# Optimization experiments

Measured on AMD Instinct MI355X. Metric: run time of the kernel, lower is better.

The kernel has to match this reference:

```python
import jax, jax.numpy as jnp
import numpy as np
from jax import lax

N = 65536          # num nodes
D_IN = 512         # in_size
H = 128            # hidden_dim
TOP_K = 8
TEMP = 1.0
CHUNK = 512        # batch_size for streaming the similarity matrix


def setup_inputs() -> dict:
    key = jax.random.key(0)
    k1, k2, k3 = jax.random.split(key, 3)
    x = jax.random.normal(k1, (N, D_IN), dtype=jnp.float32)
    # xavier-ish scale for linear weights
    s = (2.0 / (D_IN + H)) ** 0.5
    Wq = jax.random.normal(k2, (D_IN, H), dtype=jnp.float32) * s
    Wk = jax.random.normal(k3, (D_IN, H), dtype=jnp.float32) * s
    bq = jnp.zeros((H,), dtype=jnp.float32)
    bk = jnp.zeros((H,), dtype=jnp.float32)
    return {"x": x, "Wq": Wq, "bq": bq, "Wk": Wk, "bk": bk}


def reference(x, Wq, bq, Wk, bk):
    """Attention-based kNN rewiring: per-node QK similarity + top-k neighbor selection.

    Streams the [N, N] similarity matrix in row-chunks of CHUNK (mirrors the
    torch batch loop) so only a [CHUNK, N] block is live at a time.
    Returns (topk_scores [N, K], dst_indices [N, K]); src of edge e for node i
    is simply i (edge_index = stack([arange(N).repeat(K), dst.ravel()])).
    """
    q = x @ Wq + bq                      # [N, H]
    k = x @ Wk + bk                      # [N, H]
    kT = k.T                             # [H, N]
    q_chunks = q.reshape(N // CHUNK, CHUNK, H)

    def chunk_fn(qb):
        sim = (qb @ kT) / TEMP           # [CHUNK, N]
        vals, idx = lax.top_k(sim, TOP_K)  # [CHUNK, K] each
        return vals, idx

    vals, idx = lax.map(chunk_fn, q_chunks)     # [N/CHUNK, CHUNK, K]
    return vals.reshape(N, TOP_K), idx.reshape(N, TOP_K)
```

## Files before the change

### kernel.cpp

```cpp
#include <hip/hip_runtime.h>
#include <stdint.h>


#define N_NODES 65536
#define D_IN    512
#define H_DIM   128
#define TOPK    8
#define NCH     24
#define NC      48
#define CTILE   128
#define NT      (N_NODES / CTILE)
#define NTH     (NT / 2)
#define RTILE   128
#define WS_REQ  ((size_t)88080384)

typedef __attribute__((ext_vector_type(8))) int   int8v;
typedef __attribute__((ext_vector_type(4))) int   int4v;
typedef __attribute__((ext_vector_type(4))) float float4_;

__device__ __forceinline__ unsigned f2fp8(float f) {
  const unsigned u = __float_as_uint(f);
  const unsigned s = (u >> 24) & 0x80u;
  const unsigned r = u + 0x0007FFFFu + ((u >> 20) & 1u);
  const int e = (int)((r >> 23) & 0xFFu) - 127;
  const unsigned m = (r >> 20) & 7u;
  if (e < -6) {
    float a = __builtin_fabsf(f);
    unsigned q = (unsigned)(a * 512.f + 0.5f);
    if (q > 7u) q = 7u;
    return s | q;
  }
  if (e > 8 || (e == 8 && m > 6u)) return s | 0x7Eu;
  return s | ((unsigned)(e + 7) << 3) | m;
}

__device__ __forceinline__ unsigned med3u(unsigned a, unsigned b, unsigned c) {
  unsigned d;
  asm("v_med3_u32 %0, %1, %2, %3" : "=v"(d) : "v"(a), "v"(b), "v"(c));
  return d;
}

#define INS8M(T, P) do {                                                       \
    const unsigned _p = (P);                                                   \
    T[7] = med3u(_p, T[6], T[7]);                                              \
    T[6] = med3u(_p, T[5], T[6]);                                              \
    T[5] = med3u(_p, T[4], T[5]);                                              \
    T[4] = med3u(_p, T[3], T[4]);                                              \
    T[3] = med3u(_p, T[2], T[3]);                                              \
    T[2] = med3u(_p, T[1], T[2]);                                              \
    T[1] = med3u(_p, T[0], T[1]);                                              \
    T[0] = (T[0] > _p) ? T[0] : _p;                                            \
  } while (0)

__device__ __forceinline__ void gload_lds16(const void* g, void* l) {
  typedef __attribute__((address_space(1))) const unsigned int gu32;
  typedef __attribute__((address_space(3))) unsigned int lu32;
  __builtin_amdgcn_global_load_lds((gu32*)(uintptr_t)g,
                                   (lu32*)(uint32_t)(uintptr_t)l, 16, 0, 0);
}

__global__ __launch_bounds__(256) void proj_kernel(
    const float* __restrict__ x,
    const float* __restrict__ Wq, const float* __restrict__ bq,
    const float* __restrict__ Wk, const float* __restrict__ bk,
    float* __restrict__ q32, float* __restrict__ k32)
{
  const int tid = threadIdx.x;
  const int rowbase = blockIdx.x * 32;
  const int c = tid;
  const float* Wcol = (c < 128) ? (Wq + c) : (Wk + (c - 128));
  const float bias  = (c < 128) ? bq[c] : bk[c - 128];
  const float* xrow = x + (size_t)rowbase * D_IN;

  float acc[32];
  #pragma unroll
  for (int r = 0; r < 32; ++r) acc[r] = 0.f;

  for (int kc = 0; kc < D_IN; kc += 16) {
    float wv[16];
    #pragma unroll
    for (int u = 0; u < 16; ++u) wv[u] = Wcol[(size_t)(kc + u) * H_DIM];
    #pragma unroll
    for (int r = 0; r < 32; ++r) {
      #pragma unroll
      for (int u = 0; u < 16; ++u)
        acc[r] = fmaf(xrow[(size_t)r * D_IN + kc + u], wv[u], acc[r]);
    }
  }

  float* O = (c < 128) ? q32 : k32;
  const int h = c & 127;
  #pragma unroll 4
  for (int r = 0; r < 32; ++r)
    O[(size_t)(rowbase + r) * H_DIM + h] = acc[r] + bias;
}

__global__ __launch_bounds__(256) void kf8_kernel(
    const float* __restrict__ k32, unsigned char* __restrict__ Kf8)
{
  const size_t base = ((size_t)blockIdx.x * 256 + threadIdx.x) * 16;
  int d[4];
  #pragma unroll
  for (int i = 0; i < 4; ++i) {
    const float4 v = *(const float4*)(k32 + base + i * 4);
    d[i] = (int)(f2fp8(v.x) | (f2fp8(v.y) << 8) |
                 (f2fp8(v.z) << 16) | (f2fp8(v.w) << 24));
  }
  *(int4v*)(Kf8 + base) = (int4v){d[0], d[1], d[2], d[3]};
}

__global__ __launch_bounds__(256, 2) void sim_topk_f8m_kernel(
    const float* __restrict__ q32, const unsigned char* __restrict__ Kf8,
    int* __restrict__ cand)
{
  __shared__ __align__(16) char smem[32768];

  const int tid  = threadIdx.x;
  const int lane = tid & 63;
  const int w    = tid >> 6;
  const int rgrp = lane >> 4;
  const int c16  = lane & 15;
  const int rowbase = (blockIdx.x >> 1) * RTILE;
  const int chalf   = blockIdx.x & 1;
  const int tbase   = chalf * NTH;

  int8v afr[2];
  #pragma unroll
  for (int m = 0; m < 2; ++m) {
    const float* qr = q32 + (size_t)(rowbase + w * 32 + m * 16 + c16) * H_DIM
                      + rgrp * 32;
    int8v a;
    #pragma unroll
    for (int d = 0; d < 8; ++d) {
      const float4 v = *(const float4*)(qr + d * 4);
      a[d] = (int)(f2fp8(v.x) | (f2fp8(v.y) << 8) |
                   (f2fp8(v.z) << 16) | (f2fp8(v.w) << 24));
    }
    afr[m] = a;
  }

  unsigned tp[8][8];
  #pragma unroll
  for (int ri = 0; ri < 8; ++ri)
    #pragma unroll
    for (int s = 0; s < 8; ++s) tp[ri][s] = 0u;

  int rxor[2];
  #pragma unroll
  for (int j = 0; j < 2; ++j)
    rxor[j] = ((rgrp * 2 + j) ^ (c16 & 7)) << 4;

  int srcoff[4];
  #pragma unroll
  for (int j = 0; j < 4; ++j) {
    const int L  = (w * 4 + j) * 1024 + lane * 16;
    const int rr = L >> 7;
    const int sp = (L >> 4) & 7;
    srcoff[j] = rr * 128 + (((sp ^ (rr & 7))) << 4);
  }

  const char* kbytes = (const char*)Kf8;
  auto STAGE = [&](int t, int sel) {
    const char* src = kbytes + (size_t)(tbase + t) * (CTILE * 128);
    char* dst = smem + sel * 16384;
    #pragma unroll
    for (int j = 0; j < 4; ++j)
      gload_lds16(src + srcoff[j], dst + (w * 4 + j) * 1024);
  };

  STAGE(0, 0);
  __syncthreads();

  #pragma unroll 1
  for (int t = 0; t < NTH; ++t) {
    const int cur = t & 1;
    if (t + 1 < NTH) STAGE(t + 1, cur ^ 1);

    const char* kbase = smem + cur * 16384;
    #pragma unroll
    for (int f = 0; f < 8; ++f) {
      const char* rowp = kbase + (f * 16 + c16) * 128;
      const int4v lo = *(const int4v*)(rowp + rxor[0]);
      const int4v hi = *(const int4v*)(rowp + rxor[1]);
      int8v b;
      b[0] = lo[0]; b[1] = lo[1]; b[2] = lo[2]; b[3] = lo[3];
      b[4] = hi[0]; b[5] = hi[1]; b[6] = hi[2]; b[7] = hi[3];

      float4_ a0 = (float4_){0.f, 0.f, 0.f, 0.f};
      float4_ a1 = (float4_){0.f, 0.f, 0.f, 0.f};
      a0 = __builtin_amdgcn_mfma_scale_f32_16x16x128_f8f6f4(
               afr[0], b, a0, 0, 0, 0, 0x7F7F7F7F, 0, 0x7F7F7F7F);
      a1 = __builtin_amdgcn_mfma_scale_f32_16x16x128_f8f6f4(
               afr[1], b, a1, 0, 0, 0, 0x7F7F7F7F, 0, 0x7F7F7F7F);

      const unsigned colb = (unsigned)(t * CTILE + f * 16 + c16);
      #pragma unroll
      for (int r2 = 0; r2 < 4; ++r2) {
        const unsigned p0 =
            (__float_as_uint(fmaxf(a0[r2], 0.f)) & 0xFFFF0000u) | colb;
        INS8M(tp[r2], p0);
        const unsigned p1 =
            (__float_as_uint(fmaxf(a1[r2], 0.f)) & 0xFFFF0000u) | colb;
        INS8M(tp[4 + r2], p1);
      }
    }
    __syncthreads();
  }

  unsigned* pairs = (unsigned*)smem;
  const int colbase = tbase * CTILE;
  for (int p = 0; p < 4; ++p) {
    if (w == p) {
      #pragma unroll
      for (int ri = 0; ri < 8; ++ri) {
        const int rl = (ri >> 2) * 16 + rgrp * 4 + (ri & 3);
        #pragma unroll
        for (int s = 0; s < 8; ++s)
          pairs[((size_t)rl * 16 + c16) * 8 + s] = tp[ri][s];
      }
    }
    __syncthreads();
    if (tid < 32) {
      const int row = rowbase + p * 32 + tid;
      int cur[16];
      #pragma unroll
      for (int l = 0; l < 16; ++l) cur[l] = 0;
      for (int it = 0; it < NCH; ++it) {
        unsigned best = 0u; int bl = 0;
        #pragma unroll
        for (int l = 0; l < 16; ++l) {
          const int cq = cur[l] < 8 ? cur[l] : 7;
          const unsigned v =
              (cur[l] < 8) ? pairs[((size_t)tid * 16 + l) * 8 + cq] : 0u;
          if (v > best) { best = v; bl = l; }
        }
        cand[(size_t)row * NC + chalf * NCH + it] =
            colbase + (int)(best & 0xFFFFu);
        #pragma unroll
        for (int l = 0; l < 16; ++l) cur[l] += (l == bl) ? 1 : 0;
      }
    }
    __syncthreads();
  }
}

__global__ __launch_bounds__(256) void rescore48w_kernel(
    const float* __restrict__ q32, const float* __restrict__ k32,
    const int* __restrict__ cand, float* __restrict__ out)
{
  const int tid  = threadIdx.x;
  const int lane = tid & 63;
  const int w    = tid >> 6;
  const int rowbase = blockIdx.x * 8;

  #pragma unroll 1
  for (int rr = 0; rr < 2; ++rr) {
    const int row = rowbase + w * 2 + rr;
    float bs = -3.4e38f;
    int   bi = 0x7FFFFFFF;
    if (lane < NC) {
      const int ci = cand[(size_t)row * NC + lane] & (N_NODES - 1);
      const float4* qp = (const float4*)(q32 + (size_t)row * H_DIM);
      const float4* kp = (const float4*)(k32 + (size_t)ci * H_DIM);
      float s = 0.f;
      #pragma unroll 8
      for (int h4 = 0; h4 < H_DIM / 4; ++h4) {
        const float4 a = qp[h4], b = kp[h4];
        s = fmaf(a.x, b.x, s); s = fmaf(a.y, b.y, s);
        s = fmaf(a.z, b.z, s); s = fmaf(a.w, b.w, s);
      }
      bs = s;
      bi = ci;
    }
    #pragma unroll
    for (int o = 0; o < TOPK; ++o) {
      float rs = bs; int ri = bi;
      #pragma unroll
      for (int off = 32; off > 0; off >>= 1) {
        const float os = __shfl_xor(rs, off);
        const int   oi = __shfl_xor(ri, off);
        if (os > rs || (os == rs && oi < ri)) { rs = os; ri = oi; }
      }
      if (lane == 0) {
        out[(size_t)row * TOPK + o] = rs;
        out[(size_t)N_NODES * TOPK + (size_t)row * TOPK + o] = (float)ri;
      }
      if (bs == rs && bi == ri) bs = -3.4e38f;
    }
  }
}

__global__ void sentinel_kernel(float* __restrict__ out) {
  const int i = blockIdx.x * 256 + threadIdx.x;
  out[i] = 0.0f;
  out[(size_t)N_NODES * TOPK + i] = 7777.0f;
}

extern "C" void kernel_launch(void* const* d_in, const int* in_sizes, int n_in,
                              void* d_out, int out_size, void* d_ws, size_t ws_size,
                              hipStream_t stream) {
  const float* x  = (const float*)d_in[0];
  const float* Wq = (const float*)d_in[1];
  const float* bq = (const float*)d_in[2];
  const float* Wk = (const float*)d_in[3];
  const float* bk = (const float*)d_in[4];
  float* out = (float*)d_out;

  if (ws_size < WS_REQ) {
    sentinel_kernel<<<N_NODES * TOPK / 256, 256, 0, stream>>>(out);
    return;
  }

  float* q32 = (float*)d_ws;
  float* k32 = q32 + (size_t)N_NODES * H_DIM;
  int* cand  = (int*)((char*)d_ws + (size_t)67108864);
  unsigned char* Kf8 = (unsigned char*)d_ws + (size_t)79691776;

  proj_kernel<<<N_NODES / 32, 256, 0, stream>>>(x, Wq, bq, Wk, bk, q32, k32);
  kf8_kernel<<<(N_NODES * H_DIM / 16) / 256, 256, 0, stream>>>(k32, Kf8);
  sim_topk_f8m_kernel<<<N_NODES / RTILE * 2, 256, 0, stream>>>(q32, Kf8, cand);
  rescore48w_kernel<<<N_NODES / 8, 256, 0, stream>>>(q32, k32, cand, out);
}
```

Baseline: 2.659 ms.

## Pair adjacent column fragments via max before top-k insert, rescore both members

The similarity kernel now computes two 16-column MFMA fragments, takes the elementwise max of each column pair, and inserts only that max (tagged with a pair id) into the per-thread top-8. This halves the insertion-sort work in the hot loop. The rescore kernel expands each of the 48 candidate pairs back into two columns and rescores 96 candidates per row in fp32, using one wave per row. The cost is twice the exact rescore work and possible loss of recall when both members of a pair are true neighbours.

```diff
diff --git a/kernel.cpp b/kernel.cpp
--- a/kernel.cpp
+++ b/kernel.cpp
@@ -109,7 +109,7 @@
   *(int4v*)(Kf8 + base) = (int4v){d[0], d[1], d[2], d[3]};
 }
 
-__global__ __launch_bounds__(256, 2) void sim_topk_f8m_kernel(
+__global__ __launch_bounds__(256, 2) void sim_topk_f8pr_kernel(
     const float* __restrict__ q32, const unsigned char* __restrict__ Kf8,
     int* __restrict__ cand)
 {
@@ -178,29 +178,43 @@
 
     const char* kbase = smem + cur * 16384;
     #pragma unroll
-    for (int f = 0; f < 8; ++f) {
-      const char* rowp = kbase + (f * 16 + c16) * 128;
-      const int4v lo = *(const int4v*)(rowp + rxor[0]);
-      const int4v hi = *(const int4v*)(rowp + rxor[1]);
-      int8v b;
-      b[0] = lo[0]; b[1] = lo[1]; b[2] = lo[2]; b[3] = lo[3];
-      b[4] = hi[0]; b[5] = hi[1]; b[6] = hi[2]; b[7] = hi[3];
-
-      float4_ a0 = (float4_){0.f, 0.f, 0.f, 0.f};
-      float4_ a1 = (float4_){0.f, 0.f, 0.f, 0.f};
-      a0 = __builtin_amdgcn_mfma_scale_f32_16x16x128_f8f6f4(
-               afr[0], b, a0, 0, 0, 0, 0x7F7F7F7F, 0, 0x7F7F7F7F);
-      a1 = __builtin_amdgcn_mfma_scale_f32_16x16x128_f8f6f4(
-               afr[1], b, a1, 0, 0, 0, 0x7F7F7F7F, 0, 0x7F7F7F7F);
-
-      const unsigned colb = (unsigned)(t * CTILE + f * 16 + c16);
+    for (int fp = 0; fp < 4; ++fp) {
+      const char* rowp0 = kbase + ((2 * fp) * 16 + c16) * 128;
+      const int4v lo0 = *(const int4v*)(rowp0 + rxor[0]);
+      const int4v hi0 = *(const int4v*)(rowp0 + rxor[1]);
+      int8v b0;
+      b0[0] = lo0[0]; b0[1] = lo0[1]; b0[2] = lo0[2]; b0[3] = lo0[3];
+      b0[4] = hi0[0]; b0[5] = hi0[1]; b0[6] = hi0[2]; b0[7] = hi0[3];
+      float4_ a0x = (float4_){0.f, 0.f, 0.f, 0.f};
+      float4_ a1x = (float4_){0.f, 0.f, 0.f, 0.f};
+      a0x = __builtin_amdgcn_mfma_scale_f32_16x16x128_f8f6f4(
+                afr[0], b0, a0x, 0, 0, 0, 0x7F7F7F7F, 0, 0x7F7F7F7F);
+      a1x = __builtin_amdgcn_mfma_scale_f32_16x16x128_f8f6f4(
+                afr[1], b0, a1x, 0, 0, 0, 0x7F7F7F7F, 0, 0x7F7F7F7F);
+
+      const char* rowp1 = kbase + ((2 * fp + 1) * 16 + c16) * 128;
+      const int4v lo1 = *(const int4v*)(rowp1 + rxor[0]);
+      const int4v hi1 = *(const int4v*)(rowp1 + rxor[1]);
+      int8v b1;
+      b1[0] = lo1[0]; b1[1] = lo1[1]; b1[2] = lo1[2]; b1[3] = lo1[3];
+      b1[4] = hi1[0]; b1[5] = hi1[1]; b1[6] = hi1[2]; b1[7] = hi1[3];
+      float4_ a0y = (float4_){0.f, 0.f, 0.f, 0.f};
+      float4_ a1y = (float4_){0.f, 0.f, 0.f, 0.f};
+      a0y = __builtin_amdgcn_mfma_scale_f32_16x16x128_f8f6f4(
+                afr[0], b1, a0y, 0, 0, 0, 0x7F7F7F7F, 0, 0x7F7F7F7F);
+      a1y = __builtin_amdgcn_mfma_scale_f32_16x16x128_f8f6f4(
+                afr[1], b1, a1y, 0, 0, 0, 0x7F7F7F7F, 0, 0x7F7F7F7F);
+
+      const unsigned pid = (unsigned)(t * 64 + fp * 16 + c16);
       #pragma unroll
       for (int r2 = 0; r2 < 4; ++r2) {
+        const float m0 = fmaxf(a0x[r2], a0y[r2]);
         const unsigned p0 =
-            (__float_as_uint(fmaxf(a0[r2], 0.f)) & 0xFFFF0000u) | colb;
+            (__float_as_uint(fmaxf(m0, 0.f)) & 0xFFFF0000u) | pid;
         INS8M(tp[r2], p0);
+        const float m1 = fmaxf(a1x[r2], a1y[r2]);
         const unsigned p1 =
-            (__float_as_uint(fmaxf(a1[r2], 0.f)) & 0xFFFF0000u) | colb;
+            (__float_as_uint(fmaxf(m1, 0.f)) & 0xFFFF0000u) | pid;
         INS8M(tp[4 + r2], p1);
       }
     }
@@ -208,7 +222,6 @@
   }
 
   unsigned* pairs = (unsigned*)smem;
-  const int colbase = tbase * CTILE;
   for (int p = 0; p < 4; ++p) {
     if (w == p) {
       #pragma unroll
@@ -235,7 +248,7 @@
           if (v > best) { best = v; bl = l; }
         }
         cand[(size_t)row * NC + chalf * NCH + it] =
-            colbase + (int)(best & 0xFFFFu);
+            (chalf << 14) | (int)(best & 0x3FFFu);
         #pragma unroll
         for (int l = 0; l < 16; ++l) cur[l] += (l == bl) ? 1 : 0;
       }
@@ -244,24 +257,30 @@
   }
 }
 
-__global__ __launch_bounds__(256) void rescore48w_kernel(
+__global__ __launch_bounds__(256) void rescore96w_kernel(
     const float* __restrict__ q32, const float* __restrict__ k32,
     const int* __restrict__ cand, float* __restrict__ out)
 {
   const int tid  = threadIdx.x;
   const int lane = tid & 63;
   const int w    = tid >> 6;
-  const int rowbase = blockIdx.x * 8;
-
-  #pragma unroll 1
-  for (int rr = 0; rr < 2; ++rr) {
-    const int row = rowbase + w * 2 + rr;
-    float bs = -3.4e38f;
-    int   bi = 0x7FFFFFFF;
-    if (lane < NC) {
-      const int ci = cand[(size_t)row * NC + lane] & (N_NODES - 1);
-      const float4* qp = (const float4*)(q32 + (size_t)row * H_DIM);
-      const float4* kp = (const float4*)(k32 + (size_t)ci * H_DIM);
+  const int row  = blockIdx.x * 4 + w;
+
+  const float4* qp = (const float4*)(q32 + (size_t)row * H_DIM);
+
+  float s0 = -3.4e38f, s1 = -3.4e38f;
+  int   c0 = -1,       c1 = -1;
+
+  #pragma unroll
+  for (int sl = 0; sl < 2; ++sl) {
+    const int j = lane + sl * 64;
+    if (j < 2 * NC && (sl == 0 || lane < 2 * NC - 64)) {
+      const int gpid = cand[(size_t)row * NC + (j >> 1)];
+      const int ch = (gpid >> 14) & 1, pl = gpid & 16383;
+      const int tt = pl >> 6, rr = pl & 63;
+      const int colA = ch * 32768 + tt * 128 + ((rr >> 4) << 5) + (rr & 15);
+      const int col  = colA + (j & 1) * 16;
+      const float4* kp = (const float4*)(k32 + (size_t)col * H_DIM);
       float s = 0.f;
       #pragma unroll 8
       for (int h4 = 0; h4 < H_DIM / 4; ++h4) {
@@ -269,24 +288,27 @@
         s = fmaf(a.x, b.x, s); s = fmaf(a.y, b.y, s);
         s = fmaf(a.z, b.z, s); s = fmaf(a.w, b.w, s);
       }
-      bs = s;
-      bi = ci;
-    }
-    #pragma unroll
-    for (int o = 0; o < TOPK; ++o) {
-      float rs = bs; int ri = bi;
-      #pragma unroll
-      for (int off = 32; off > 0; off >>= 1) {
-        const float os = __shfl_xor(rs, off);
-        const int   oi = __shfl_xor(ri, off);
-        if (os > rs || (os == rs && oi < ri)) { rs = os; ri = oi; }
-      }
-      if (lane == 0) {
-        out[(size_t)row * TOPK + o] = rs;
-        out[(size_t)N_NODES * TOPK + (size_t)row * TOPK + o] = (float)ri;
-      }
-      if (bs == rs && bi == ri) bs = -3.4e38f;
-    }
+      if (sl == 0) { s0 = s; c0 = col; } else { s1 = s; c1 = col; }
+    }
+  }
+
+  #pragma unroll
+  for (int o = 0; o < TOPK; ++o) {
+    float ls; int lc;
+    if (s0 > s1 || (s0 == s1 && (unsigned)c0 < (unsigned)c1)) { ls = s0; lc = c0; }
+    else                                                      { ls = s1; lc = c1; }
+    #pragma unroll
+    for (int off = 32; off > 0; off >>= 1) {
+      const float os = __shfl_xor(ls, off);
+      const int   oc = __shfl_xor(lc, off);
+      if (os > ls || (os == ls && (unsigned)oc < (unsigned)lc)) { ls = os; lc = oc; }
+    }
+    if (lane == 0) {
+      out[(size_t)row * TOPK + o] = ls;
+      out[(size_t)N_NODES * TOPK + (size_t)row * TOPK + o] = (float)lc;
+    }
+    if (lc == c0) s0 = -3.4e38f;
+    if (lc == c1) s1 = -3.4e38f;
   }
 }
 
@@ -318,6 +340,6 @@
 
   proj_kernel<<<N_NODES / 32, 256, 0, stream>>>(x, Wq, bq, Wk, bk, q32, k32);
   kf8_kernel<<<(N_NODES * H_DIM / 16) / 256, 256, 0, stream>>>(k32, Kf8);
-  sim_topk_f8m_kernel<<<N_NODES / RTILE * 2, 256, 0, stream>>>(q32, Kf8, cand);
-  rescore48w_kernel<<<N_NODES / 8, 256, 0, stream>>>(q32, k32, cand, out);
-}
+  sim_topk_f8pr_kernel<<<N_NODES / RTILE * 2, 256, 0, stream>>>(q32, Kf8, cand);
+  rescore96w_kernel<<<N_NODES / 4, 256, 0, stream>>>(q32, k32, cand, out);
+}
```

Measured after the change: 2.288 ms. -14.0%, faster.
